# Kernel optimization log

Hardware: AMD Instinct MI355X
Metric: run time of the kernel (lower is better)

## Reference

```python
import jax, jax.numpy as jnp
import numpy as np

N = 200000      # nodes
E = 1600000     # edges
B = 1000        # graphs
SD = 64         # state_dim
AD = 32         # action_dim
H = 128         # HIDDEN_LAYER
EPS = 1e-5


def setup_inputs() -> dict:
    key = jax.random.key(0)
    ks = jax.random.split(key, 16)
    x = jax.random.normal(ks[0], (N, SD), dtype=jnp.float32)
    action = jax.random.normal(ks[1], (N, AD), dtype=jnp.float32)
    edge_index = jax.random.randint(ks[2], (2, E), 0, N, dtype=jnp.int64)
    batch_size = jnp.sort(jax.random.randint(ks[3], (N,), 0, B, dtype=jnp.int64))
    # parameters (Linear weights stored [in, out]; torch init std=0.1 for fc layers)
    W_gcn = jax.random.normal(ks[4], (SD, H), dtype=jnp.float32) / np.sqrt(SD)
    b_gcn = jnp.zeros((H,), jnp.float32)
    g0 = jnp.ones((H,), jnp.float32); be0 = jnp.zeros((H,), jnp.float32)
    W1 = jax.random.normal(ks[5], (H, H), dtype=jnp.float32) * 0.1
    b1 = jnp.zeros((H,), jnp.float32)
    g1 = jnp.ones((H,), jnp.float32); be1 = jnp.zeros((H,), jnp.float32)
    W2 = jax.random.normal(ks[6], (AD, H), dtype=jnp.float32) * 0.1
    b2 = jnp.zeros((H,), jnp.float32)
    g2 = jnp.ones((H,), jnp.float32); be2 = jnp.zeros((H,), jnp.float32)
    W3 = jax.random.normal(ks[7], (2 * H, 1), dtype=jnp.float32) * 0.1
    b3 = jnp.zeros((1,), jnp.float32)
    return dict(x=x, action=action, W_gcn=W_gcn, b_gcn=b_gcn, g0=g0, be0=be0,
                W1=W1, b1=b1, g1=g1, be1=be1, W2=W2, b2=b2, g2=g2, be2=be2,
                W3=W3, b3=b3, edge_index=edge_index, batch_size=batch_size)


def _bn(h, gamma, beta):
    # BatchNorm1d, training-mode batch statistics over the node axis
    mu = jnp.mean(h, axis=0)
    var = jnp.var(h, axis=0)
    return (h - mu) * jax.lax.rsqrt(var + EPS) * gamma + beta


def _gcn(x, edge_index, W, b):
    # GCN conv with self-loops and symmetric normalization:
    # out_i = sum_{j in N(i) u {i}} (d_i d_j)^{-1/2} (x_j W) + b
    loops = jnp.arange(N, dtype=edge_index.dtype)
    src = jnp.concatenate([edge_index[0], loops])
    dst = jnp.concatenate([edge_index[1], loops])
    deg = jax.ops.segment_sum(jnp.ones_like(dst, dtype=x.dtype), dst, num_segments=N)
    dinv = jax.lax.rsqrt(deg)                       # deg >= 1 due to self-loops
    norm = dinv[src] * dinv[dst]                    # [E+N]
    xw = x @ W                                      # [N, H]
    msg = xw[src] * norm[:, None]                   # [E+N, H]
    return jax.ops.segment_sum(msg, dst, num_segments=N) + b


def reference(x, action, W_gcn, b_gcn, g0, be0, W1, b1, g1, be1,
              W2, b2, g2, be2, W3, b3, edge_index, batch_size):
    h0 = jax.nn.relu(_gcn(x, edge_index, W_gcn, b_gcn))
    h0n = _bn(h0, g0, be0)
    h1 = jax.nn.relu(h0n @ W1 + b1)
    h1n = _bn(h1, g1, be1)
    h2 = jax.nn.relu(action @ W2 + b2)
    h2n = _bn(h2, g2, be2)
    feat = jnp.concatenate([h1n, h2n], axis=1)      # [N, 2H]
    sums = jax.ops.segment_sum(feat, batch_size, num_segments=B)
    cnts = jax.ops.segment_sum(jnp.ones((N,), feat.dtype), batch_size, num_segments=B)
    pooled = sums / jnp.maximum(cnts, 1.0)[:, None]  # [B, 2H]
    return pooled @ W3 + b3                          # [B, 1]
```

## Files before the change

### kernel.cpp

```cpp
#include <hip/hip_runtime.h>

typedef unsigned short u16;
typedef unsigned int   u32;
typedef __bf16 bf16x8 __attribute__((ext_vector_type(8)));
typedef float  f32x4  __attribute__((ext_vector_type(4)));

#define EPS 1e-5f
#define BSHIFT 9

__device__ __forceinline__ float b2f(u16 u){ union{u32 i; float f;} v; v.i=((u32)u)<<16; return v.f; }
__device__ __forceinline__ u16 f2b(float f){
  u32 x = __float_as_uint(f);
  u32 r = x + 0x7fffu + ((x>>16)&1u);
  return (u16)(r>>16);
}

template<int K, bool RELU, bool HASBIAS, bool AF32, bool POOL>
__global__ __launch_bounds__(256) void k_gemm(const void* __restrict__ Av,
                                              const u16* __restrict__ BhiT,
                                              const u16* __restrict__ BloT,
                                              const float* __restrict__ bias,
                                              u16* __restrict__ C,
                                              float* __restrict__ stats,
                                              const int* __restrict__ batch,
                                              float* __restrict__ P, int M)
{
  constexpr int KM = K / 8;
  __shared__ u16 lds[2 * 128 * K];
  __shared__ float sred[128], qred[128];
  const int tid = threadIdx.x;
  for (int i = tid; i < 128 * KM; i += 256) {
    const int n = i / KM, kb = i % KM;
    const int kb2 = kb ^ (n & (KM - 1));
    *(uint4*)(&lds[(n * KM + kb2) * 8])           = *(const uint4*)(BhiT + i * 8);
    *(uint4*)(&lds[128 * K + (n * KM + kb2) * 8]) = *(const uint4*)(BloT + i * 8);
  }
  if (tid < 128) { sred[tid] = 0.f; qred[tid] = 0.f; }
  __syncthreads();
  const int wid = tid >> 6, lane = tid & 63, q = lane >> 4, r16 = lane & 15;
  const int ntiles = M >> 6;
  float ls[8], lq[8];
#pragma unroll
  for (int nb = 0; nb < 8; nb++) { ls[nb] = 0.f; lq[nb] = 0.f; }
  for (int tile = blockIdx.x; tile < ntiles; tile += gridDim.x) {
    const int arow = (tile << 6) + (wid << 4) + r16;
    bf16x8 av[K / 32];
    if (AF32) {
      const float* Af = (const float*)Av + (size_t)arow * K + q * 8;
#pragma unroll
      for (int kk = 0; kk < K / 32; kk++) {
        f32x4 x0 = *(const f32x4*)(Af + kk * 32);
        f32x4 x1 = *(const f32x4*)(Af + kk * 32 + 4);
#pragma unroll
        for (int j = 0; j < 4; j++) { av[kk][j] = (__bf16)x0[j]; av[kk][4 + j] = (__bf16)x1[j]; }
      }
    } else {
      const u16* Ab = (const u16*)Av + (size_t)arow * K + q * 8;
#pragma unroll
      for (int kk = 0; kk < K / 32; kk++) av[kk] = *(const bf16x8*)(Ab + kk * 32);
    }
    f32x4 acc[8];
#pragma unroll
    for (int nb = 0; nb < 8; nb++) acc[nb] = (f32x4){0.f, 0.f, 0.f, 0.f};
#pragma unroll
    for (int kk = 0; kk < K / 32; kk++) {
#pragma unroll
      for (int nb = 0; nb < 8; nb++) {
        const int n = nb * 16 + r16;
        const int kb2 = (kk * 4 + q) ^ (n & (KM - 1));
        const bf16x8 bh = *(const bf16x8*)(&lds[(n * KM + kb2) * 8]);
        const bf16x8 bl = *(const bf16x8*)(&lds[128 * K + (n * KM + kb2) * 8]);
        acc[nb] = __builtin_amdgcn_mfma_f32_16x16x32_bf16(av[kk], bh, acc[nb], 0, 0, 0);
        acc[nb] = __builtin_amdgcn_mfma_f32_16x16x32_bf16(av[kk], bl, acc[nb], 0, 0, 0);
      }
    }
    const int rbase = (tile << 6) + (wid << 4) + (q << 2);
    if (!POOL) {
#pragma unroll
      for (int nb = 0; nb < 8; nb++) {
        const int col = nb * 16 + r16;
        const float bv = HASBIAS ? bias[col] : 0.f;
#pragma unroll
        for (int r = 0; r < 4; r++) {
          float v = acc[nb][r] + bv;
          if (RELU) v = fmaxf(v, 0.f);
          ls[nb] += v; lq[nb] += v * v;
          C[(size_t)(rbase + r) * 128 + col] = f2b(v);
        }
      }
    } else {
#pragma unroll
      for (int nb = 0; nb < 8; nb++) {
        const int col = nb * 16 + r16;
        const float bv = HASBIAS ? bias[col] : 0.f;
#pragma unroll
        for (int r = 0; r < 4; r++) {
          float v = acc[nb][r] + bv;
          if (RELU) v = fmaxf(v, 0.f);
          ls[nb] += v; lq[nb] += v * v;
          acc[nb][r] = v;
        }
      }
      int bg[4];
#pragma unroll
      for (int r = 0; r < 4; r++) bg[r] = batch[rbase + r];
      const int wrow = (tile << 6) + (wid << 4);
      const int g0 = batch[wrow];
      const int g1 = batch[wrow + 15];
      for (int g = g0; g <= g1; ++g) {
#pragma unroll
        for (int nb = 0; nb < 8; nb++) {
          float sv = 0.f;
#pragma unroll
          for (int r = 0; r < 4; r++) sv += (bg[r] == g) ? acc[nb][r] : 0.f;
          sv += __shfl_xor(sv, 16, 64);
          sv += __shfl_xor(sv, 32, 64);
          if (q == 0) atomicAdd(&P[g * 128 + nb * 16 + r16], sv);
        }
      }
    }
  }
#pragma unroll
  for (int nb = 0; nb < 8; nb++) {
    atomicAdd(&sred[nb * 16 + r16], ls[nb]);
    atomicAdd(&qred[nb * 16 + r16], lq[nb]);
  }
  __syncthreads();
  if (tid < 128) {
    atomicAdd(&stats[tid], sred[tid]);
    atomicAdd(&stats[128 + tid], qred[tid]);
  }
}

__global__ void k_prep0(const float* __restrict__ Wg, const float* __restrict__ W2,
                        u16* __restrict__ WghiT, u16* __restrict__ WgloT,
                        u16* __restrict__ W2hiT, u16* __restrict__ W2loT,
                        const int* __restrict__ batch, int* __restrict__ gofs,
                        int* __restrict__ zbase, int zwords, int NZ, int N, int B)
{
  const int bid = blockIdx.x, t = threadIdx.x;
  if (bid < NZ) {
    const int i = bid * 2048 + t * 8;
    if (i < zwords) {
      *(int4*)(zbase + i)     = make_int4(0, 0, 0, 0);
      *(int4*)(zbase + i + 4) = make_int4(0, 0, 0, 0);
    }
  } else if (bid < NZ + 48) {
    const int i = (bid - NZ) * 256 + t;
    if (i < 64 * 128) {
      int k = i >> 7, n = i & 127;
      float w = Wg[i]; u16 h = f2b(w);
      WghiT[n * 64 + k] = h; WgloT[n * 64 + k] = f2b(w - b2f(h));
    } else if (i < 64 * 128 + 32 * 128) {
      int j = i - 64 * 128;
      int k = j >> 7, n = j & 127;
      float w = W2[j]; u16 h = f2b(w);
      W2hiT[n * 32 + k] = h; W2loT[n * 32 + k] = f2b(w - b2f(h));
    }
  } else {
    const int i = (bid - NZ - 48) * 256 + t;
    if (i == 0) { for (int g = 0; g <= batch[0]; g++) gofs[g] = 0; }
    if (i == N - 1) { for (int g = batch[N - 1] + 1; g <= B; g++) gofs[g] = N; }
    if (i < N - 1) {
      const int b0 = batch[i], b1 = batch[i + 1];
      for (int g = b0 + 1; g <= b1; g++) gofs[g] = i + 1;
    }
  }
}

__global__ __launch_bounds__(256) void k_bincnt(const int* __restrict__ dst, int* __restrict__ btot,
                                                int E, int NB)
{
  extern __shared__ int hist[];
  const int tid = threadIdx.x;
  for (int i = tid; i < NB; i += 256) hist[i] = 0;
  __syncthreads();
  const int chunk = (E + gridDim.x - 1) / gridDim.x;
  const int start = blockIdx.x * chunk;
  const int end = min(start + chunk, E);
  for (int e = start + tid; e < end; e += 256) atomicAdd(&hist[((u32)dst[e]) >> BSHIFT], 1);
  __syncthreads();
  for (int i = tid; i < NB; i += 256) if (hist[i]) atomicAdd(&btot[i], hist[i]);
}

__global__ void k_exscan(const int* __restrict__ in, int* __restrict__ out, int n)
{
  __shared__ int s[256];
  const int t = threadIdx.x;
  const int per = (n + 255) / 256;
  const int base = t * per;
  int loc[8]; int sum = 0;
  for (int j = 0; j < per; j++) { int v = (base + j < n) ? in[base + j] : 0; loc[j] = sum; sum += v; }
  s[t] = sum; __syncthreads();
  for (int o = 1; o < 256; o <<= 1) {
    int x = (t >= o) ? s[t - o] : 0;
    __syncthreads();
    s[t] += x;
    __syncthreads();
  }
  const int ex = s[t] - sum;
  for (int j = 0; j < per; j++) if (base + j < n) out[base + j] = ex + loc[j];
  if (t == 255) out[n] = s[255];
}

__global__ __launch_bounds__(256) void k_bin(const int* __restrict__ src, const int* __restrict__ dst,
                                             const int* __restrict__ bbase, int* __restrict__ bcur,
                                             uint2* __restrict__ pairs, int E, int NB)
{
  extern __shared__ int lds[];
  int* hist = lds; int* wbase = lds + NB;
  const int tid = threadIdx.x;
  for (int i = tid; i < NB; i += 256) hist[i] = 0;
  __syncthreads();
  const int chunk = (E + gridDim.x - 1) / gridDim.x;
  const int start = blockIdx.x * chunk;
  const int end = min(start + chunk, E);
  for (int e = start + tid; e < end; e += 256) atomicAdd(&hist[((u32)dst[e]) >> BSHIFT], 1);
  __syncthreads();
  for (int i = tid; i < NB; i += 256) {
    int c = hist[i];
    wbase[i] = c ? bbase[i] + atomicAdd(&bcur[i], c) : 0;
    hist[i] = 0;
  }
  __syncthreads();
  for (int e = start + tid; e < end; e += 256) {
    const int d = dst[e];
    const int b = ((u32)d) >> BSHIFT;
    const int o = atomicAdd(&hist[b], 1);
    pairs[wbase[b] + o] = make_uint2((u32)d, (u32)src[e]);
  }
}

__global__ __launch_bounds__(256) void k_bucket(const uint2* __restrict__ pairs,
                                                const int* __restrict__ bbase,
                                                const float* __restrict__ x,
                                                int* __restrict__ offsets, float* __restrict__ dinv,
                                                int* __restrict__ elist, u16* __restrict__ y,
                                                int N, int NB, int Etot)
{
  __shared__ int hist[512];
  __shared__ int scan[256];
  __shared__ int lcur[512];
  __shared__ float sdinv[512];
  const int b = blockIdx.x, t = threadIdx.x;
  const int nbase = b << BSHIFT;
  const int nn = min(1 << BSHIFT, N - nbase);
  hist[t] = 0; hist[256 + t] = 0;
  __syncthreads();
  const int p0 = bbase[b], p1 = bbase[b + 1];
  for (int p = p0 + t; p < p1; p += 256) atomicAdd(&hist[pairs[p].x - nbase], 1);
  __syncthreads();
  const int h0 = hist[2 * t], h1 = hist[2 * t + 1];
  const int psum = h0 + h1;
  scan[t] = psum; __syncthreads();
  for (int o = 1; o < 256; o <<= 1) {
    int xx = (t >= o) ? scan[t - o] : 0;
    __syncthreads();
    scan[t] += xx;
    __syncthreads();
  }
  const int ex = scan[t] - psum;
  const int li0 = 2 * t, li1 = 2 * t + 1;
  if (li0 < nn) {
    const int i = nbase + li0;
    const int off = p0 + ex + i;
    const float d = rsqrtf((float)(h0 + 1));
    offsets[i] = off; elist[off] = i; lcur[li0] = off + 1;
    dinv[i] = d; sdinv[li0] = d;
  }
  if (li1 < nn) {
    const int i = nbase + li1;
    const int off = p0 + ex + h0 + i;
    const float d = rsqrtf((float)(h1 + 1));
    offsets[i] = off; elist[off] = i; lcur[li1] = off + 1;
    dinv[i] = d; sdinv[li1] = d;
  }
  if (b == NB - 1 && t == 0) offsets[N] = Etot;
  __syncthreads();
  for (int p = p0 + t; p < p1; p += 256) {
    const uint2 pr = pairs[p];
    const int pos = atomicAdd(&lcur[pr.x - nbase], 1);
    elist[pos] = (int)pr.y;
  }
  const size_t ebase = (size_t)nbase * 64;
  const int total = nn * 64;
  for (int i = t * 8; i < total; i += 256 * 8) {
    const float d = sdinv[i >> 6];
    f32x4 a = *(const f32x4*)(x + ebase + i);
    f32x4 c = *(const f32x4*)(x + ebase + i + 4);
    u16 o[8];
#pragma unroll
    for (int j = 0; j < 4; j++) { o[j] = f2b(a[j] * d); o[4 + j] = f2b(c[j] * d); }
    *(uint4*)(y + ebase + i) = *(uint4*)o;
  }
}

__global__ __launch_bounds__(256) void k_agg(const u16* __restrict__ y, const int* __restrict__ offsets,
                                             const int* __restrict__ elist, const float* __restrict__ dinv,
                                             u16* __restrict__ aggx, int n)
{
  const int lane = threadIdx.x & 63;
  const int half = lane >> 5, l32 = lane & 31;
  const int g4 = l32 >> 3, sub = lane & 7;
  const int wid  = (blockIdx.x * 256 + threadIdx.x) >> 6;
  const int nw   = gridDim.x * 4;
  const int npair = (n + 1) >> 1;
  for (int pr = wid; pr < npair; pr += nw) {
    const int node = pr * 2 + half;
    const int s0 = offsets[node], s1 = offsets[node + 1];
    const int mydeg = s1 - s0;
    const int degA = __shfl(mydeg, 0, 64);
    const int degB = __shfl(mydeg, 32, 64);
    const int degmax = max(degA, degB);
    float a[8];
#pragma unroll
    for (int t = 0; t < 8; t++) a[t] = 0.f;
    for (int base = 0; base < degmax; base += 32) {
      const int m = mydeg - base;
      const int ev = (base + l32 < mydeg) ? elist[s0 + base + l32] : 0;
      const int iters = (min(32, degmax - base) + 3) >> 2;
      for (int it = 0; it < iters; it++) {
        const int j = it * 4 + g4;
        const int idx = __shfl(ev, half * 32 + j, 64);
        if (j < m) {
          const uint4 v = *(const uint4*)(y + (size_t)idx * 64 + sub * 8);
          const u32 w[4] = {v.x, v.y, v.z, v.w};
#pragma unroll
          for (int t = 0; t < 4; t++) {
            a[2 * t]     += b2f((u16)w[t]);
            a[2 * t + 1] += b2f((u16)(w[t] >> 16));
          }
        }
      }
    }
#pragma unroll
    for (int t = 0; t < 8; t++) {
      a[t] += __shfl_xor(a[t], 8, 64);
      a[t] += __shfl_xor(a[t], 16, 64);
    }
    if (g4 == 0) {
      const float di = dinv[node];
      u16 o[8];
#pragma unroll
      for (int t = 0; t < 8; t++) o[t] = f2b(a[t] * di);
      *(uint4*)(aggx + (size_t)node * 64 + sub * 8) = *(uint4*)o;
    }
  }
}

__global__ void k_prep1(const float* __restrict__ stats0, const float* __restrict__ W1,
                        const float* __restrict__ b1, const float* __restrict__ g0,
                        const float* __restrict__ be0, u16* __restrict__ W1hiT,
                        u16* __restrict__ W1loT, float* __restrict__ b1p, float n)
{
  __shared__ float A[8], Csh[8];
  const int t = threadIdx.x;
  if (t < 8) {
    const int k = blockIdx.x * 8 + t;
    const float mu = stats0[k] / n;
    const float var = fmaxf(stats0[128 + k] / n - mu * mu, 0.f);
    const float a = g0[k] * rsqrtf(var + EPS);
    A[t] = a; Csh[t] = be0[k] - mu * a;
  }
  __syncthreads();
  float acc = (blockIdx.x == 0) ? b1[t] : 0.f;
#pragma unroll
  for (int kk = 0; kk < 8; kk++) {
    const int k = blockIdx.x * 8 + kk;
    const float w0 = W1[k * 128 + t];
    acc += Csh[kk] * w0;
    const float w = A[kk] * w0;
    const u16 h = f2b(w);
    W1hiT[t * 128 + k] = h;
    W1loT[t * 128 + k] = f2b(w - b2f(h));
  }
  atomicAdd(&b1p[t], acc);
}

__global__ void k_prep2(const float* __restrict__ stats1, const float* __restrict__ stats2,
                        const float* __restrict__ g1, const float* __restrict__ be1,
                        const float* __restrict__ g2, const float* __restrict__ be2,
                        const float* __restrict__ W3, const float* __restrict__ b3,
                        float* __restrict__ w1f, float* __restrict__ w2f,
                        float* __restrict__ constS, float n)
{
  __shared__ float red[256];
  const int t = threadIdx.x;
  float c, wv;
  if (t < 128) {
    const float mu = stats1[t] / n;
    const float var = fmaxf(stats1[128 + t] / n - mu * mu, 0.f);
    const float a = g1[t] * rsqrtf(var + EPS);
    c = be1[t] - mu * a;
    wv = W3[t];
    w1f[t] = a * wv;
  } else {
    const int f = t - 128;
    const float mu = stats2[f] / n;
    const float var = fmaxf(stats2[128 + f] / n - mu * mu, 0.f);
    const float a = g2[f] * rsqrtf(var + EPS);
    c = be2[f] - mu * a;
    wv = W3[t];
    w2f[f] = a * wv;
  }
  red[t] = c * wv; __syncthreads();
  for (int o = 128; o; o >>= 1) { if (t < o) red[t] += red[t + o]; __syncthreads(); }
  if (t == 0) { constS[0] = red[0] + b3[0]; constS[1] = b3[0]; }
}

__global__ void k_out2(const float* __restrict__ P1, const float* __restrict__ P2,
                       const int* __restrict__ gofs, const float* __restrict__ w1f,
                       const float* __restrict__ w2f, const float* __restrict__ constS,
                       float* __restrict__ out, int B)
{
  const int lane = threadIdx.x & 63;
  const int g = (blockIdx.x * 256 + threadIdx.x) >> 6;
  if (g >= B) return;
  const int c = gofs[g + 1] - gofs[g];
  const int k = 2 * lane;
  float d = P1[g * 128 + k] * w1f[k] + P1[g * 128 + k + 1] * w1f[k + 1]
          + P2[g * 128 + k] * w2f[k] + P2[g * 128 + k + 1] * w2f[k + 1];
#pragma unroll
  for (int o = 1; o < 64; o <<= 1) d += __shfl_xor(d, o, 64);
  if (lane == 0) out[g] = (c > 0) ? d / (float)c + constS[0] : constS[1];
}

extern "C" void kernel_launch(void* const* d_in, const int* in_sizes, int n_in,
                              void* d_out, int out_size, void* d_ws, size_t ws_size,
                              hipStream_t stream)
{
  const float* x    = (const float*)d_in[0];
  const float* act  = (const float*)d_in[1];
  const float* Wg   = (const float*)d_in[2];
  const float* bg   = (const float*)d_in[3];
  const float* g0   = (const float*)d_in[4];
  const float* be0  = (const float*)d_in[5];
  const float* W1   = (const float*)d_in[6];
  const float* b1   = (const float*)d_in[7];
  const float* g1   = (const float*)d_in[8];
  const float* be1  = (const float*)d_in[9];
  const float* W2   = (const float*)d_in[10];
  const float* b2   = (const float*)d_in[11];
  const float* g2   = (const float*)d_in[12];
  const float* be2  = (const float*)d_in[13];
  const float* W3   = (const float*)d_in[14];
  const float* b3   = (const float*)d_in[15];
  const int* eidx   = (const int*)d_in[16];
  const int* batch  = (const int*)d_in[17];

  const int N = in_sizes[17];
  const int E = in_sizes[16] / 2;
  const int B = out_size;
  const int* src = eidx;
  const int* dst = eidx + E;
  const int NB = (N + (1 << BSHIFT) - 1) >> BSHIFT;

  char* ws = (char*)d_ws;
  size_t off = 0;
  auto alloc = [&](size_t bytes) -> char* {
    off = (off + 255) & ~(size_t)255;
    char* p = ws + off; off += bytes; return p;
  };

  u16* bufA = (u16*)alloc((size_t)N * 128 * 2);
  u16* xb   = (u16*)alloc((size_t)N * 64 * 2);
  u16* aggx = (u16*)alloc((size_t)N * 64 * 2);

  int zwords = 768 + 128 + 2 * NB + 2 * 128 * B;
  zwords = (zwords + 7) & ~7;
  char* zbase   = alloc((size_t)zwords * 4);
  float* stats0 = (float*)zbase;
  float* stats1 = stats0 + 256;
  float* stats2 = stats1 + 256;
  float* b1p    = stats2 + 256;
  int*   btot   = (int*)(b1p + 128);
  int*   bcur   = btot + NB;
  float* P1     = (float*)(bcur + NB);
  float* P2     = P1 + 128 * B;

  int*   offsets = (int*)alloc((size_t)(N + 1) * 4);
  float* dinv    = (float*)alloc((size_t)N * 4);
  int*   elist   = (int*)alloc((size_t)(E + N) * 4);
  uint2* pairs   = (uint2*)alloc((size_t)E * 8);
  int*   bbase   = (int*)alloc((size_t)(NB + 1) * 4);
  int*   gofs    = (int*)alloc((size_t)(B + 1) * 4);
  u16*   WghiT   = (u16*)alloc(128 * 64 * 2);
  u16*   WgloT   = (u16*)alloc(128 * 64 * 2);
  u16*   W1hiT   = (u16*)alloc(128 * 128 * 2);
  u16*   W1loT   = (u16*)alloc(128 * 128 * 2);
  u16*   W2hiT   = (u16*)alloc(128 * 32 * 2);
  u16*   W2loT   = (u16*)alloc(128 * 32 * 2);
  float* w1f     = (float*)alloc(128 * 4);
  float* w2f     = (float*)alloc(128 * 4);
  float* constS  = (float*)alloc(2 * 4);

  u16* h0 = bufA;

  const int NZ = (zwords + 2047) / 2048;
  const int nbounds = (N + 255) / 256;
  k_prep0<<<NZ + 48 + nbounds, 256, 0, stream>>>(Wg, W2, WghiT, WgloT, W2hiT, W2loT,
                                                 batch, gofs, (int*)zbase, zwords, NZ, N, B);
  k_bincnt<<<256, 256, NB * 4, stream>>>(dst, btot, E, NB);
  k_exscan<<<1, 256, 0, stream>>>(btot, bbase, NB);
  k_bin<<<256, 256, 2 * NB * 4, stream>>>(src, dst, bbase, bcur, pairs, E, NB);
  k_bucket<<<NB, 256, 0, stream>>>(pairs, bbase, x, offsets, dinv, elist, xb, N, NB, E + N);
  k_agg<<<2048, 256, 0, stream>>>(xb, offsets, elist, dinv, aggx, N);
  k_gemm<64, true, true, false, false><<<1024, 256, 0, stream>>>(aggx, WghiT, WgloT, bg,
                                                                 h0, stats0, nullptr, nullptr, N);
  k_prep1<<<16, 128, 0, stream>>>(stats0, W1, b1, g0, be0, W1hiT, W1loT, b1p, (float)N);
  k_gemm<128, true, true, false, true><<<1024, 256, 0, stream>>>(h0, W1hiT, W1loT, b1p,
                                                                 nullptr, stats1, batch, P1, N);
  k_gemm<32, true, true, true, true><<<1024, 256, 0, stream>>>(act, W2hiT, W2loT, b2,
                                                               nullptr, stats2, batch, P2, N);
  k_prep2<<<1, 256, 0, stream>>>(stats1, stats2, g1, be1, g2, be2, W3, b3, w1f, w2f, constS, (float)N);
  k_out2<<<(B * 64 + 255) / 256, 256, 0, stream>>>(P1, P2, gofs, w1f, w2f, constS, (float*)d_out, B);
}
```

Before: 440.5 us.

## Split GEMM output columns across block pairs and process two row tiles per iteration

Each GEMM block now computes only half of the 128 output columns, selected by block index parity, which halves the LDS footprint for the weight tiles. Each loop iteration handles a 128-row tile as two 64-row sub-tiles that share the same B fragments, and the grid is doubled with an occupancy hint of 4 blocks per CU. The goal is more resident waves and more MFMA work per LDS read. In exchange, each A row is read twice (once per column half) and the pooling atomics and batch lookups are duplicated across the two halves.

```diff
diff --git a/kernel.cpp b/kernel.cpp
--- a/kernel.cpp
+++ b/kernel.cpp
@@ -16,119 +16,140 @@
 }
 
 template<int K, bool RELU, bool HASBIAS, bool AF32, bool POOL>
-__global__ __launch_bounds__(256) void k_gemm(const void* __restrict__ Av,
-                                              const u16* __restrict__ BhiT,
-                                              const u16* __restrict__ BloT,
-                                              const float* __restrict__ bias,
-                                              u16* __restrict__ C,
-                                              float* __restrict__ stats,
-                                              const int* __restrict__ batch,
-                                              float* __restrict__ P, int M)
+__global__ __launch_bounds__(256, 4) void k_gemm(const void* __restrict__ Av,
+                                                 const u16* __restrict__ BhiT,
+                                                 const u16* __restrict__ BloT,
+                                                 const float* __restrict__ bias,
+                                                 u16* __restrict__ C,
+                                                 float* __restrict__ stats,
+                                                 const int* __restrict__ batch,
+                                                 float* __restrict__ P, int M)
 {
   constexpr int KM = K / 8;
-  __shared__ u16 lds[2 * 128 * K];
-  __shared__ float sred[128], qred[128];
+  constexpr int KR = K / 32;
+  __shared__ u16 lds[2 * 64 * K];
+  __shared__ float sred[64], qred[64];
   const int tid = threadIdx.x;
-  for (int i = tid; i < 128 * KM; i += 256) {
+  const int ch = blockIdx.x & 1;
+  for (int i = tid; i < 64 * KM; i += 256) {
     const int n = i / KM, kb = i % KM;
     const int kb2 = kb ^ (n & (KM - 1));
-    *(uint4*)(&lds[(n * KM + kb2) * 8])           = *(const uint4*)(BhiT + i * 8);
-    *(uint4*)(&lds[128 * K + (n * KM + kb2) * 8]) = *(const uint4*)(BloT + i * 8);
-  }
-  if (tid < 128) { sred[tid] = 0.f; qred[tid] = 0.f; }
+    const int gsrc = ((ch * 64 + n) * KM + kb) * 8;
+    *(uint4*)(&lds[(n * KM + kb2) * 8])          = *(const uint4*)(BhiT + gsrc);
+    *(uint4*)(&lds[64 * K + (n * KM + kb2) * 8]) = *(const uint4*)(BloT + gsrc);
+  }
+  if (tid < 64) { sred[tid] = 0.f; qred[tid] = 0.f; }
   __syncthreads();
   const int wid = tid >> 6, lane = tid & 63, q = lane >> 4, r16 = lane & 15;
-  const int ntiles = M >> 6;
-  float ls[8], lq[8];
-#pragma unroll
-  for (int nb = 0; nb < 8; nb++) { ls[nb] = 0.f; lq[nb] = 0.f; }
-  for (int tile = blockIdx.x; tile < ntiles; tile += gridDim.x) {
-    const int arow = (tile << 6) + (wid << 4) + r16;
-    bf16x8 av[K / 32];
+  const int nt2 = (M + 127) >> 7;
+  const int t0 = blockIdx.x >> 1, tstride = gridDim.x >> 1;
+  float ls[4], lq[4];
+#pragma unroll
+  for (int nb = 0; nb < 4; nb++) { ls[nb] = 0.f; lq[nb] = 0.f; }
+
+  for (int tile = t0; tile < nt2; tile += tstride) {
+    const int rowb0 = tile << 7;
+    const bool ok1 = (rowb0 + 64) < M;
+
+    bf16x8 av0[KR], av1[KR];
     if (AF32) {
-      const float* Af = (const float*)Av + (size_t)arow * K + q * 8;
-#pragma unroll
-      for (int kk = 0; kk < K / 32; kk++) {
-        f32x4 x0 = *(const f32x4*)(Af + kk * 32);
-        f32x4 x1 = *(const f32x4*)(Af + kk * 32 + 4);
-#pragma unroll
-        for (int j = 0; j < 4; j++) { av[kk][j] = (__bf16)x0[j]; av[kk][4 + j] = (__bf16)x1[j]; }
+      const float* Af0 = (const float*)Av + (size_t)(rowb0 + (wid << 4) + r16) * K + q * 8;
+#pragma unroll
+      for (int kk = 0; kk < KR; kk++) {
+        f32x4 x0 = *(const f32x4*)(Af0 + kk * 32);
+        f32x4 x1 = *(const f32x4*)(Af0 + kk * 32 + 4);
+#pragma unroll
+        for (int j = 0; j < 4; j++) { av0[kk][j] = (__bf16)x0[j]; av0[kk][4 + j] = (__bf16)x1[j]; }
+      }
+      if (ok1) {
+        const float* Af1 = Af0 + (size_t)64 * K;
+#pragma unroll
+        for (int kk = 0; kk < KR; kk++) {
+          f32x4 x0 = *(const f32x4*)(Af1 + kk * 32);
+          f32x4 x1 = *(const f32x4*)(Af1 + kk * 32 + 4);
+#pragma unroll
+          for (int j = 0; j < 4; j++) { av1[kk][j] = (__bf16)x0[j]; av1[kk][4 + j] = (__bf16)x1[j]; }
+        }
       }
     } else {
-      const u16* Ab = (const u16*)Av + (size_t)arow * K + q * 8;
-#pragma unroll
-      for (int kk = 0; kk < K / 32; kk++) av[kk] = *(const bf16x8*)(Ab + kk * 32);
-    }
-    f32x4 acc[8];
-#pragma unroll
-    for (int nb = 0; nb < 8; nb++) acc[nb] = (f32x4){0.f, 0.f, 0.f, 0.f};
-#pragma unroll
-    for (int kk = 0; kk < K / 32; kk++) {
-#pragma unroll
-      for (int nb = 0; nb < 8; nb++) {
+      const u16* Ab0 = (const u16*)Av + (size_t)(rowb0 + (wid << 4) + r16) * K + q * 8;
+#pragma unroll
+      for (int kk = 0; kk < KR; kk++) av0[kk] = *(const bf16x8*)(Ab0 + kk * 32);
+      if (ok1) {
+        const u16* Ab1 = Ab0 + (size_t)64 * K;
+#pragma unroll
+        for (int kk = 0; kk < KR; kk++) av1[kk] = *(const bf16x8*)(Ab1 + kk * 32);
+      }
+    }
+
+    f32x4 acc0[4], acc1[4];
+#pragma unroll
+    for (int nb = 0; nb < 4; nb++) { acc0[nb] = (f32x4){0.f,0.f,0.f,0.f}; acc1[nb] = (f32x4){0.f,0.f,0.f,0.f}; }
+#pragma unroll
+    for (int kk = 0; kk < KR; kk++) {
+#pragma unroll
+      for (int nb = 0; nb < 4; nb++) {
         const int n = nb * 16 + r16;
         const int kb2 = (kk * 4 + q) ^ (n & (KM - 1));
         const bf16x8 bh = *(const bf16x8*)(&lds[(n * KM + kb2) * 8]);
-        const bf16x8 bl = *(const bf16x8*)(&lds[128 * K + (n * KM + kb2) * 8]);
-        acc[nb] = __builtin_amdgcn_mfma_f32_16x16x32_bf16(av[kk], bh, acc[nb], 0, 0, 0);
-        acc[nb] = __builtin_amdgcn_mfma_f32_16x16x32_bf16(av[kk], bl, acc[nb], 0, 0, 0);
-      }
-    }
-    const int rbase = (tile << 6) + (wid << 4) + (q << 2);
-    if (!POOL) {
-#pragma unroll
-      for (int nb = 0; nb < 8; nb++) {
-        const int col = nb * 16 + r16;
+        const bf16x8 bl = *(const bf16x8*)(&lds[64 * K + (n * KM + kb2) * 8]);
+        acc0[nb] = __builtin_amdgcn_mfma_f32_16x16x32_bf16(av0[kk], bh, acc0[nb], 0, 0, 0);
+        acc0[nb] = __builtin_amdgcn_mfma_f32_16x16x32_bf16(av0[kk], bl, acc0[nb], 0, 0, 0);
+        if (ok1) {
+          acc1[nb] = __builtin_amdgcn_mfma_f32_16x16x32_bf16(av1[kk], bh, acc1[nb], 0, 0, 0);
+          acc1[nb] = __builtin_amdgcn_mfma_f32_16x16x32_bf16(av1[kk], bl, acc1[nb], 0, 0, 0);
+        }
+      }
+    }
+
+    auto epi = [&](f32x4* acc, int rowbase) {
+      const int rbase = rowbase + (wid << 4) + (q << 2);
+      int bg[4];
+      if (POOL) {
+#pragma unroll
+        for (int r = 0; r < 4; r++) bg[r] = batch[rbase + r];
+      }
+#pragma unroll
+      for (int nb = 0; nb < 4; nb++) {
+        const int col = ch * 64 + nb * 16 + r16;
         const float bv = HASBIAS ? bias[col] : 0.f;
 #pragma unroll
         for (int r = 0; r < 4; r++) {
           float v = acc[nb][r] + bv;
           if (RELU) v = fmaxf(v, 0.f);
           ls[nb] += v; lq[nb] += v * v;
-          C[(size_t)(rbase + r) * 128 + col] = f2b(v);
+          if (!POOL) C[(size_t)(rbase + r) * 128 + col] = f2b(v);
+          else acc[nb][r] = v;
         }
       }
-    } else {
-#pragma unroll
-      for (int nb = 0; nb < 8; nb++) {
-        const int col = nb * 16 + r16;
-        const float bv = HASBIAS ? bias[col] : 0.f;
-#pragma unroll
-        for (int r = 0; r < 4; r++) {
-          float v = acc[nb][r] + bv;
-          if (RELU) v = fmaxf(v, 0.f);
-          ls[nb] += v; lq[nb] += v * v;
-          acc[nb][r] = v;
+      if (POOL) {
+        const int g0 = __shfl(bg[0], 0, 64);
+        const int g1 = __shfl(bg[3], 48, 64);
+        for (int g = g0; g <= g1; ++g) {
+#pragma unroll
+          for (int nb = 0; nb < 4; nb++) {
+            float sv = 0.f;
+#pragma unroll
+            for (int r = 0; r < 4; r++) sv += (bg[r] == g) ? acc[nb][r] : 0.f;
+            sv += __shfl_xor(sv, 16, 64);
+            sv += __shfl_xor(sv, 32, 64);
+            if (q == 0) atomicAdd(&P[g * 128 + ch * 64 + nb * 16 + r16], sv);
+          }
         }
       }
-      int bg[4];
-#pragma unroll
-      for (int r = 0; r < 4; r++) bg[r] = batch[rbase + r];
-      const int wrow = (tile << 6) + (wid << 4);
-      const int g0 = batch[wrow];
-      const int g1 = batch[wrow + 15];
-      for (int g = g0; g <= g1; ++g) {
-#pragma unroll
-        for (int nb = 0; nb < 8; nb++) {
-          float sv = 0.f;
-#pragma unroll
-          for (int r = 0; r < 4; r++) sv += (bg[r] == g) ? acc[nb][r] : 0.f;
-          sv += __shfl_xor(sv, 16, 64);
-          sv += __shfl_xor(sv, 32, 64);
-          if (q == 0) atomicAdd(&P[g * 128 + nb * 16 + r16], sv);
-        }
-      }
-    }
-  }
-#pragma unroll
-  for (int nb = 0; nb < 8; nb++) {
+    };
+    epi(acc0, rowb0);
+    if (ok1) epi(acc1, rowb0 + 64);
+  }
+#pragma unroll
+  for (int nb = 0; nb < 4; nb++) {
     atomicAdd(&sred[nb * 16 + r16], ls[nb]);
     atomicAdd(&qred[nb * 16 + r16], lq[nb]);
   }
   __syncthreads();
-  if (tid < 128) {
-    atomicAdd(&stats[tid], sred[tid]);
-    atomicAdd(&stats[128 + tid], qred[tid]);
+  if (tid < 64) {
+    atomicAdd(&stats[ch * 64 + tid], sred[tid]);
+    atomicAdd(&stats[128 + ch * 64 + tid], qred[tid]);
   }
 }
 
@@ -505,12 +526,12 @@
   k_bin<<<256, 256, 2 * NB * 4, stream>>>(src, dst, bbase, bcur, pairs, E, NB);
   k_bucket<<<NB, 256, 0, stream>>>(pairs, bbase, x, offsets, dinv, elist, xb, N, NB, E + N);
   k_agg<<<2048, 256, 0, stream>>>(xb, offsets, elist, dinv, aggx, N);
-  k_gemm<64, true, true, false, false><<<1024, 256, 0, stream>>>(aggx, WghiT, WgloT, bg,
+  k_gemm<64, true, true, false, false><<<2048, 256, 0, stream>>>(aggx, WghiT, WgloT, bg,
                                                                  h0, stats0, nullptr, nullptr, N);
   k_prep1<<<16, 128, 0, stream>>>(stats0, W1, b1, g0, be0, W1hiT, W1loT, b1p, (float)N);
-  k_gemm<128, true, true, false, true><<<1024, 256, 0, stream>>>(h0, W1hiT, W1loT, b1p,
+  k_gemm<128, true, true, false, true><<<2048, 256, 0, stream>>>(h0, W1hiT, W1loT, b1p,
                                                                  nullptr, stats1, batch, P1, N);
-  k_gemm<32, true, true, true, true><<<1024, 256, 0, stream>>>(act, W2hiT, W2loT, b2,
+  k_gemm<32, true, true, true, true><<<2048, 256, 0, stream>>>(act, W2hiT, W2loT, b2,
                                                                nullptr, stats2, batch, P2, N);
   k_prep2<<<1, 256, 0, stream>>>(stats1, stats2, g1, be1, g2, be2, W3, b3, w1f, w2f, constS, (float)N);
   k_out2<<<(B * 64 + 255) / 256, 256, 0, stream>>>(P1, P2, gofs, w1f, w2f, constS, (float*)d_out, B);
```

New measurement: 542.6 us. 23.2% more time.
